# Kernel tuning notes

Measured on AMD Instinct MI355X. Metric: run time of the kernel, lower is better.

The kernel has to match this reference:

```python
import jax, jax.numpy as jnp
import numpy as np

V, N, K, D = 100000, 20000, 32, 128
NEG = -1e9  # masked logit value


def setup_inputs() -> dict:
    key = jax.random.key(0)
    ks = jax.random.split(key, 8)
    return {
        "nodes": jax.random.randint(ks[0], (N,), 0, V),
        "neigh_idx": jax.random.randint(ks[1], (N, K), 0, V),
        "degrees": jax.random.randint(ks[2], (N,), 0, K + 1),
        "u2e": jax.random.normal(ks[3], (V, D), dtype=jnp.float32),
        "W1": jax.random.normal(ks[4], (2 * D, D), dtype=jnp.float32) * 0.05,
        "b1": jnp.zeros((D,), jnp.float32),
        "W2": jax.random.normal(ks[5], (D, D), dtype=jnp.float32) * 0.05,
        "b2": jnp.zeros((D,), jnp.float32),
        "W3": jax.random.normal(ks[6], (D, 1), dtype=jnp.float32) * 0.05,
        "b3": jnp.zeros((1,), jnp.float32),
    }


def reference(nodes, neigh_idx, degrees, u2e, W1, b1, W2, b2, W3, b3):
    self_feats = u2e[nodes]                      # [N, D]
    e_u = u2e[neigh_idx]                         # [N, K, D] ragged gather (padded)
    # Attention MLP: cat(neighbor, self) -> relu -> relu -> scalar logit
    x = jnp.concatenate([e_u, jnp.broadcast_to(self_feats[:, None, :], (e_u.shape[0], K, D))], axis=-1)  # [N, K, 2D]
    h = jax.nn.relu(x @ W1 + b1)                 # [N, K, D]
    h = jax.nn.relu(h @ W2 + b2)                 # [N, K, D]
    logits = (h @ W3 + b3)[..., 0]               # [N, K]
    mask = jnp.arange(K)[None, :] < degrees[:, None]
    att = jax.nn.softmax(jnp.where(mask, logits, NEG), axis=-1)  # softmax over neighbors
    agg = jnp.einsum("nk,nkd->nd", att, e_u)     # attention-weighted neighbor sum
    out = jnp.where(degrees[:, None] > 0, (agg + self_feats) * 0.5, self_feats)
    return out
```

## Files before the change

kernel.cpp:

```cpp
#include <hip/hip_runtime.h>
#include <hip/hip_bf16.h>

#define KK 32
#define DD 128
#define NEGV (-1e9f)
#define SE 136

typedef __attribute__((ext_vector_type(8))) short bf16x8;
typedef __attribute__((ext_vector_type(4))) float f32x4;

__device__ __forceinline__ unsigned short f2bf(float f) {
    union { float f; unsigned u; } v; v.f = f;
    unsigned r = v.u + 0x7fffu + ((v.u >> 16) & 1u);
    return (unsigned short)(r >> 16);
}
__device__ __forceinline__ float bf2f(unsigned short h) {
    union { unsigned u; float f; } v; v.u = ((unsigned)h) << 16;
    return v.f;
}
__device__ __forceinline__ unsigned pk2(float x, float y) {
    union { __hip_bfloat162 h; unsigned u; } c;
    c.h = __float22bfloat162_rn(float2{x, y});
    return c.u;
}

__global__ __launch_bounds__(256) void prep_kernel(
    const float* __restrict__ u2e, const float* __restrict__ W1, const float* __restrict__ W2,
    unsigned short* __restrict__ u2e_bf, unsigned short* __restrict__ W1t,
    unsigned short* __restrict__ W2t, const int u2e_blocks)
{
    const int b = blockIdx.x;
    if (b < u2e_blocks) {
        const long base = (long)b * 2048 + threadIdx.x * 8;
        const float4* s = (const float4*)(u2e + base);
        const float4 v0 = s[0], v1 = s[1];
        uint4 p;
        p.x = pk2(v0.x, v0.y); p.y = pk2(v0.z, v0.w);
        p.z = pk2(v1.x, v1.y); p.w = pk2(v1.z, v1.w);
        *(uint4*)(u2e_bf + base) = p;
    } else {
        const int id = (b - u2e_blocks) * 256 + threadIdx.x;
        if (id < 256 * 128) {
            const int n = id >> 8, k = id & 255;
            W1t[id] = f2bf(W1[k * DD + n]);
        } else {
            const int j = id - 256 * 128;
            const int n = j >> 7, k = j & 127;
            W2t[j] = f2bf(W2[k * DD + n]);
        }
    }
}

template<bool BF>
__global__ __launch_bounds__(256, 2) void ppagg_mfma(
    const int* __restrict__ nodes, const int* __restrict__ neigh,
    const int* __restrict__ degrees, const float* __restrict__ u2e,
    const unsigned short* __restrict__ u2e_bf,
    const unsigned short* __restrict__ W1t, const unsigned short* __restrict__ W2t,
    const float* __restrict__ b1, const float* __restrict__ b2,
    const float* __restrict__ W3, const float* __restrict__ b3,
    float* __restrict__ out, const int Nn)
{
    __shared__ __align__(16) unsigned short s_eh[128 * SE];
    __shared__ __align__(16) unsigned short s_x[4 * DD];
    __shared__ float s_part[4][128];
    __shared__ float s_att[128];
    __shared__ int   s_idx[256];

    const int tid  = threadIdx.x;
    const int w    = tid >> 6;
    const int lane = tid & 63;
    const int ln   = lane & 15;
    const int q    = lane >> 4;

    bf16x8 b1f[8][2], b2f[4][2];
    float b1c[2], b2c[2], w3c[2];
    const int c0 = w * 32 + ln;
    const int c1 = c0 + 16;
    #pragma unroll
    for (int kk = 0; kk < 8; ++kk) {
        b1f[kk][0] = *(const bf16x8*)(W1t + c0 * 256 + kk * 32 + q * 8);
        b1f[kk][1] = *(const bf16x8*)(W1t + c1 * 256 + kk * 32 + q * 8);
    }
    #pragma unroll
    for (int kk = 0; kk < 4; ++kk) {
        b2f[kk][0] = *(const bf16x8*)(W2t + c0 * 128 + kk * 32 + q * 8);
        b2f[kk][1] = *(const bf16x8*)(W2t + c1 * 128 + kk * 32 + q * 8);
    }
    b1c[0] = b1[c0]; b1c[1] = b1[c1];
    b2c[0] = b2[c0]; b2c[1] = b2[c1];
    w3c[0] = W3[c0]; w3c[1] = W3[c1];

    const int nb = blockIdx.x * 8;
    const int r  = tid & 127;
    const int h  = tid >> 7;

    int idxA, idxB;
    {
        int ng0 = nb + (r >> 5);       if (ng0 >= Nn) ng0 = Nn - 1;
        int ng1 = nb + 4 + (r >> 5);   if (ng1 >= Nn) ng1 = Nn - 1;
        idxA = neigh[ng0 * KK + (r & 31)];
        idxB = neigh[ng1 * KK + (r & 31)];
    }
    float2 self0, self1;
    {
        int n0 = nb + w;       if (n0 >= Nn) n0 = Nn - 1;
        int n1 = nb + 4 + w;   if (n1 >= Nn) n1 = Nn - 1;
        self0 = *(const float2*)(u2e + (long)nodes[n0] * DD + lane * 2);
        self1 = *(const float2*)(u2e + (long)nodes[n1] * DD + lane * 2);
    }

    #pragma unroll
    for (int it = 0; it < 2; ++it) {
        const int gbase = nb + it * 4;
        const float2 selfv = it ? self1 : self0;
        const int myidx = it ? idxB : idxA;

        {
            unsigned short* dst = s_eh + r * SE + h * 64;
            if (BF) {
                const uint4* src = (const uint4*)(u2e_bf + (long)myidx * DD + h * 64);
                #pragma unroll
                for (int c = 0; c < 8; ++c) *(uint4*)(dst + c * 8) = src[c];
            } else {
                const float4* src = (const float4*)(u2e + (long)myidx * DD + h * 64);
                #pragma unroll
                for (int c8 = 0; c8 < 8; ++c8) {
                    const float4 v0 = src[c8 * 2];
                    const float4 v1 = src[c8 * 2 + 1];
                    uint4 p;
                    p.x = pk2(v0.x, v0.y); p.y = pk2(v0.z, v0.w);
                    p.z = pk2(v1.x, v1.y); p.w = pk2(v1.z, v1.w);
                    *(uint4*)(dst + c8 * 8) = p;
                }
            }
            *(unsigned*)(s_x + w * DD + lane * 2) = pk2(selfv.x, selfv.y);
            if (it == 0 && h == 0) { s_idx[r] = idxA; s_idx[128 + r] = idxB; }
        }
        __syncthreads();

        f32x4 acc[8][2];
        #pragma unroll
        for (int mt = 0; mt < 8; ++mt) {
            acc[mt][0] = (f32x4){0.f, 0.f, 0.f, 0.f};
            acc[mt][1] = (f32x4){0.f, 0.f, 0.f, 0.f};
        }
        #pragma unroll
        for (int kk = 0; kk < 4; ++kk) {
            bf16x8 a[8];
            #pragma unroll
            for (int mt = 0; mt < 8; ++mt)
                a[mt] = *(const bf16x8*)(s_eh + (mt * 16 + ln) * SE + kk * 32 + q * 8);
            #pragma unroll
            for (int mt = 0; mt < 8; ++mt) {
                acc[mt][0] = __builtin_amdgcn_mfma_f32_16x16x32_bf16(a[mt], b1f[kk][0], acc[mt][0], 0, 0, 0);
                acc[mt][1] = __builtin_amdgcn_mfma_f32_16x16x32_bf16(a[mt], b1f[kk][1], acc[mt][1], 0, 0, 0);
            }
        }
        #pragma unroll
        for (int kk = 4; kk < 8; ++kk) {
            #pragma unroll
            for (int mt = 0; mt < 8; ++mt) {
                const bf16x8 a = *(const bf16x8*)(s_x + (mt >> 1) * DD + (kk - 4) * 32 + q * 8);
                acc[mt][0] = __builtin_amdgcn_mfma_f32_16x16x32_bf16(a, b1f[kk][0], acc[mt][0], 0, 0, 0);
                acc[mt][1] = __builtin_amdgcn_mfma_f32_16x16x32_bf16(a, b1f[kk][1], acc[mt][1], 0, 0, 0);
            }
        }
        __syncthreads();

        #pragma unroll
        for (int mt = 0; mt < 8; ++mt)
            #pragma unroll
            for (int nt = 0; nt < 2; ++nt) {
                const int c = nt ? c1 : c0;
                #pragma unroll
                for (int rr = 0; rr < 4; rr += 2) {
                    const unsigned p = pk2(fmaxf(acc[mt][nt][rr]     + b1c[nt], 0.f),
                                           fmaxf(acc[mt][nt][rr + 1] + b1c[nt], 0.f));
                    const int row = mt * 16 + q * 4 + rr;
                    s_eh[row * SE + c]       = (unsigned short)(p & 0xffffu);
                    s_eh[(row + 1) * SE + c] = (unsigned short)(p >> 16);
                }
            }
        __syncthreads();

        f32x4 acc2[8][2];
        #pragma unroll
        for (int mt = 0; mt < 8; ++mt) {
            acc2[mt][0] = (f32x4){0.f, 0.f, 0.f, 0.f};
            acc2[mt][1] = (f32x4){0.f, 0.f, 0.f, 0.f};
        }
        #pragma unroll
        for (int kk = 0; kk < 4; ++kk) {
            bf16x8 a[8];
            #pragma unroll
            for (int mt = 0; mt < 8; ++mt)
                a[mt] = *(const bf16x8*)(s_eh + (mt * 16 + ln) * SE + kk * 32 + q * 8);
            #pragma unroll
            for (int mt = 0; mt < 8; ++mt) {
                acc2[mt][0] = __builtin_amdgcn_mfma_f32_16x16x32_bf16(a[mt], b2f[kk][0], acc2[mt][0], 0, 0, 0);
                acc2[mt][1] = __builtin_amdgcn_mfma_f32_16x16x32_bf16(a[mt], b2f[kk][1], acc2[mt][1], 0, 0, 0);
            }
        }
        #pragma unroll
        for (int mt = 0; mt < 8; ++mt) {
            float p[4];
            #pragma unroll
            for (int rr = 0; rr < 4; ++rr) {
                const float h0 = fmaxf(acc2[mt][0][rr] + b2c[0], 0.f);
                const float h1v = fmaxf(acc2[mt][1][rr] + b2c[1], 0.f);
                p[rr] = fmaf(h0, w3c[0], h1v * w3c[1]);
            }
            #pragma unroll
            for (int off = 1; off < 16; off <<= 1) {
                #pragma unroll
                for (int rr = 0; rr < 4; ++rr) p[rr] += __shfl_xor(p[rr], off);
            }
            if (ln == 0) {
                const int row0 = mt * 16 + q * 4;
                #pragma unroll
                for (int rr = 0; rr < 4; ++rr) s_part[w][row0 + rr] = p[rr];
            }
        }
        __syncthreads();

        if (tid < 128) {
            const int row = tid;
            const float logit = s_part[0][row] + s_part[1][row] + s_part[2][row] + s_part[3][row] + b3[0];
            int ng = gbase + (row >> 5);
            if (ng >= Nn) ng = Nn - 1;
            const int deg = degrees[ng];
            const float ml = ((row & 31) < deg) ? logit : NEGV;
            float mx = ml;
            #pragma unroll
            for (int off = 16; off > 0; off >>= 1) mx = fmaxf(mx, __shfl_xor(mx, off));
            const float e = __expf(ml - mx);
            float ssum = e;
            #pragma unroll
            for (int off = 16; off > 0; off >>= 1) ssum += __shfl_xor(ssum, off);
            s_att[row] = e / ssum;
        }
        __syncthreads();

        {
            const int ng = gbase + w;
            float ax = 0.f, ay = 0.f;
            #pragma unroll
            for (int k = 0; k < KK; ++k) {
                const float a    = s_att[w * KK + k];
                const int   ridx = s_idx[it * 128 + w * KK + k];
                if (BF) {
                    const unsigned pe = *(const unsigned*)(u2e_bf + (long)ridx * DD + lane * 2);
                    ax = fmaf(a, bf2f((unsigned short)(pe & 0xffffu)), ax);
                    ay = fmaf(a, bf2f((unsigned short)(pe >> 16)), ay);
                } else {
                    const float2 ev = *(const float2*)(u2e + (long)ridx * DD + lane * 2);
                    ax = fmaf(a, ev.x, ax);
                    ay = fmaf(a, ev.y, ay);
                }
            }
            if (ng < Nn) {
                const int deg = degrees[ng];
                float2 o;
                o.x = (deg > 0) ? 0.5f * (ax + selfv.x) : selfv.x;
                o.y = (deg > 0) ? 0.5f * (ay + selfv.y) : selfv.y;
                *(float2*)(out + (long)ng * DD + lane * 2) = o;
            }
        }
    }
}

extern "C" void kernel_launch(void* const* d_in, const int* in_sizes, int n_in,
                              void* d_out, int out_size, void* d_ws, size_t ws_size,
                              hipStream_t stream) {
    const int*   nodes   = (const int*)d_in[0];
    const int*   neigh   = (const int*)d_in[1];
    const int*   degrees = (const int*)d_in[2];
    const float* u2e     = (const float*)d_in[3];
    const float* W1      = (const float*)d_in[4];
    const float* b1      = (const float*)d_in[5];
    const float* W2      = (const float*)d_in[6];
    const float* b2      = (const float*)d_in[7];
    const float* W3      = (const float*)d_in[8];
    const float* b3      = (const float*)d_in[9];
    float* out = (float*)d_out;

    const int  Nn = in_sizes[0];
    const long Vd = (long)in_sizes[3];

    unsigned short* W1t = (unsigned short*)d_ws;
    unsigned short* W2t = W1t + 256 * 128;
    unsigned short* u2e_bf = W2t + 128 * 128;

    const size_t need_bf = (size_t)(256 * 128 + 128 * 128) * 2 + (size_t)Vd * 2;
    const bool use_bf = (ws_size >= need_bf) && (Vd % 2048 == 0);
    const int u2e_blocks = use_bf ? (int)(Vd / 2048) : 0;

    prep_kernel<<<u2e_blocks + 192, 256, 0, stream>>>(u2e, W1, W2, u2e_bf, W1t, W2t, u2e_blocks);

    const int grid = (Nn + 7) / 8;
    if (use_bf)
        ppagg_mfma<true><<<grid, 256, 0, stream>>>(nodes, neigh, degrees, u2e, u2e_bf,
                                                   W1t, W2t, b1, b2, W3, b3, out, Nn);
    else
        ppagg_mfma<false><<<grid, 256, 0, stream>>>(nodes, neigh, degrees, u2e, nullptr,
                                                    W1t, W2t, b1, b2, W3, b3, out, Nn);
}
```

Baseline: 216.6 us.

## Make MFMA aggregation kernel persistent with prefetch of next unit's indices

Replaces the fixed two-iteration-per-block scheme with a grid-stride persistent loop over 4-node units, capped at 1024 blocks. The neighbor indices and self features for the next unit are loaded into registers while the current unit's MLP runs, and double-buffered shared index storage keeps them separate. This amortizes the per-block weight-fragment loads into registers across many units and hides index-load latency. In exchange, the grid size is fixed, so load balance and occupancy now depend on the 1024 cap, and the loop is no longer unrolled.

```diff
diff --git a/kernel.cpp b/kernel.cpp
--- a/kernel.cpp
+++ b/kernel.cpp
@@ -65,7 +65,7 @@
     __shared__ __align__(16) unsigned short s_x[4 * DD];
     __shared__ float s_part[4][128];
     __shared__ float s_att[128];
-    __shared__ int   s_idx[256];
+    __shared__ int   s_idx[2][128];
 
     const int tid  = threadIdx.x;
     const int w    = tid >> 6;
@@ -91,39 +91,33 @@
     b2c[0] = b2[c0]; b2c[1] = b2[c1];
     w3c[0] = W3[c0]; w3c[1] = W3[c1];
 
-    const int nb = blockIdx.x * 8;
     const int r  = tid & 127;
     const int h  = tid >> 7;
 
-    int idxA, idxB;
+    const int units = (Nn + 3) / 4;
+    int u = blockIdx.x;
+
+    int idx_cur; float2 self_cur;
     {
-        int ng0 = nb + (r >> 5);       if (ng0 >= Nn) ng0 = Nn - 1;
-        int ng1 = nb + 4 + (r >> 5);   if (ng1 >= Nn) ng1 = Nn - 1;
-        idxA = neigh[ng0 * KK + (r & 31)];
-        idxB = neigh[ng1 * KK + (r & 31)];
-    }
-    float2 self0, self1;
-    {
-        int n0 = nb + w;       if (n0 >= Nn) n0 = Nn - 1;
-        int n1 = nb + 4 + w;   if (n1 >= Nn) n1 = Nn - 1;
-        self0 = *(const float2*)(u2e + (long)nodes[n0] * DD + lane * 2);
-        self1 = *(const float2*)(u2e + (long)nodes[n1] * DD + lane * 2);
-    }
-
-    #pragma unroll
-    for (int it = 0; it < 2; ++it) {
-        const int gbase = nb + it * 4;
-        const float2 selfv = it ? self1 : self0;
-        const int myidx = it ? idxB : idxA;
+        const int uc = (u < units) ? u : (units - 1);
+        int ng = uc * 4 + (r >> 5); if (ng >= Nn) ng = Nn - 1;
+        idx_cur = neigh[ng * KK + (r & 31)];
+        int ns = uc * 4 + w; if (ns >= Nn) ns = Nn - 1;
+        self_cur = *(const float2*)(u2e + (long)nodes[ns] * DD + lane * 2);
+    }
+
+    int par = 0;
+    for (; u < units; u += gridDim.x, par ^= 1) {
+        const int gbase = u * 4;
 
         {
             unsigned short* dst = s_eh + r * SE + h * 64;
             if (BF) {
-                const uint4* src = (const uint4*)(u2e_bf + (long)myidx * DD + h * 64);
+                const uint4* src = (const uint4*)(u2e_bf + (long)idx_cur * DD + h * 64);
                 #pragma unroll
                 for (int c = 0; c < 8; ++c) *(uint4*)(dst + c * 8) = src[c];
             } else {
-                const float4* src = (const float4*)(u2e + (long)myidx * DD + h * 64);
+                const float4* src = (const float4*)(u2e + (long)idx_cur * DD + h * 64);
                 #pragma unroll
                 for (int c8 = 0; c8 < 8; ++c8) {
                     const float4 v0 = src[c8 * 2];
@@ -134,10 +128,21 @@
                     *(uint4*)(dst + c8 * 8) = p;
                 }
             }
-            *(unsigned*)(s_x + w * DD + lane * 2) = pk2(selfv.x, selfv.y);
-            if (it == 0 && h == 0) { s_idx[r] = idxA; s_idx[128 + r] = idxB; }
-        }
-        __syncthreads();
+            *(unsigned*)(s_x + w * DD + lane * 2) = pk2(self_cur.x, self_cur.y);
+            if (h == 0) s_idx[par][r] = idx_cur;
+        }
+        __syncthreads();
+
+        int idx_next = idx_cur; float2 self_next = self_cur;
+        {
+            const int un = u + gridDim.x;
+            if (un < units) {
+                int ng = un * 4 + (r >> 5); if (ng >= Nn) ng = Nn - 1;
+                idx_next = neigh[ng * KK + (r & 31)];
+                int ns = un * 4 + w; if (ns >= Nn) ns = Nn - 1;
+                self_next = *(const float2*)(u2e + (long)nodes[ns] * DD + lane * 2);
+            }
+        }
 
         f32x4 acc[8][2];
         #pragma unroll
@@ -207,7 +212,7 @@
             float p[4];
             #pragma unroll
             for (int rr = 0; rr < 4; ++rr) {
-                const float h0 = fmaxf(acc2[mt][0][rr] + b2c[0], 0.f);
+                const float h0  = fmaxf(acc2[mt][0][rr] + b2c[0], 0.f);
                 const float h1v = fmaxf(acc2[mt][1][rr] + b2c[1], 0.f);
                 p[rr] = fmaf(h0, w3c[0], h1v * w3c[1]);
             }
@@ -248,7 +253,7 @@
             #pragma unroll
             for (int k = 0; k < KK; ++k) {
                 const float a    = s_att[w * KK + k];
-                const int   ridx = s_idx[it * 128 + w * KK + k];
+                const int   ridx = s_idx[par][w * KK + k];
                 if (BF) {
                     const unsigned pe = *(const unsigned*)(u2e_bf + (long)ridx * DD + lane * 2);
                     ax = fmaf(a, bf2f((unsigned short)(pe & 0xffffu)), ax);
@@ -262,11 +267,12 @@
             if (ng < Nn) {
                 const int deg = degrees[ng];
                 float2 o;
-                o.x = (deg > 0) ? 0.5f * (ax + selfv.x) : selfv.x;
-                o.y = (deg > 0) ? 0.5f * (ay + selfv.y) : selfv.y;
+                o.x = (deg > 0) ? 0.5f * (ax + self_cur.x) : self_cur.x;
+                o.y = (deg > 0) ? 0.5f * (ay + self_cur.y) : self_cur.y;
                 *(float2*)(out + (long)ng * DD + lane * 2) = o;
             }
         }
+        idx_cur = idx_next; self_cur = self_next;
     }
 }
 
@@ -298,7 +304,8 @@
 
     prep_kernel<<<u2e_blocks + 192, 256, 0, stream>>>(u2e, W1, W2, u2e_bf, W1t, W2t, u2e_blocks);
 
-    const int grid = (Nn + 7) / 8;
+    const int units = (Nn + 3) / 4;
+    const int grid  = units < 1024 ? units : 1024;
     if (use_bf)
         ppagg_mfma<true><<<grid, 256, 0, stream>>>(nodes, neigh, degrees, u2e, u2e_bf,
                                                    W1t, W2t, b1, b2, W3, b3, out, Nn);
```

Measured after the change: 235.2 us. 1.09x slower.

## Repartition second MLP layer per wave so softmax needs no cross-wave reduction

Applied to the files above, without the earlier changes.

Layer 2 is re-tiled so each wave computes all 128 output columns for the 32 neighbor rows of its own node, instead of a 32-column slice across all 128 rows. The logit dot product with W3 and the masked softmax can then finish inside one wave, which removes the shared partial-sum buffer and two block-wide barriers. Degrees are also loaded once up front rather than re-read. In exchange, W2 fragments are now read from global/L2 on every k-step instead of being held in registers. That frees VGPRs but adds load latency and traffic inside the MFMA loop.

```diff
diff --git a/kernel.cpp b/kernel.cpp
--- a/kernel.cpp
+++ b/kernel.cpp
@@ -63,9 +63,9 @@
 {
     __shared__ __align__(16) unsigned short s_eh[128 * SE];
     __shared__ __align__(16) unsigned short s_x[4 * DD];
-    __shared__ float s_part[4][128];
-    __shared__ float s_att[128];
-    __shared__ int   s_idx[256];
+    __shared__ float s_l[4][32];
+    __shared__ float s_att[4][32];
+    __shared__ int   s_idx[2][128];
 
     const int tid  = threadIdx.x;
     const int w    = tid >> 6;
@@ -73,8 +73,8 @@
     const int ln   = lane & 15;
     const int q    = lane >> 4;
 
-    bf16x8 b1f[8][2], b2f[4][2];
-    float b1c[2], b2c[2], w3c[2];
+    bf16x8 b1f[8][2];
+    float b1c[2];
     const int c0 = w * 32 + ln;
     const int c1 = c0 + 16;
     #pragma unroll
@@ -82,14 +82,14 @@
         b1f[kk][0] = *(const bf16x8*)(W1t + c0 * 256 + kk * 32 + q * 8);
         b1f[kk][1] = *(const bf16x8*)(W1t + c1 * 256 + kk * 32 + q * 8);
     }
+    b1c[0] = b1[c0]; b1c[1] = b1[c1];
+    float b2c8[8], w3c8[8];
     #pragma unroll
-    for (int kk = 0; kk < 4; ++kk) {
-        b2f[kk][0] = *(const bf16x8*)(W2t + c0 * 128 + kk * 32 + q * 8);
-        b2f[kk][1] = *(const bf16x8*)(W2t + c1 * 128 + kk * 32 + q * 8);
-    }
-    b1c[0] = b1[c0]; b1c[1] = b1[c1];
-    b2c[0] = b2[c0]; b2c[1] = b2[c1];
-    w3c[0] = W3[c0]; w3c[1] = W3[c1];
+    for (int nt = 0; nt < 8; ++nt) {
+        b2c8[nt] = b2[nt * 16 + ln];
+        w3c8[nt] = W3[nt * 16 + ln];
+    }
+    const float b3c = b3[0];
 
     const int nb = blockIdx.x * 8;
     const int r  = tid & 127;
@@ -103,11 +103,13 @@
         idxB = neigh[ng1 * KK + (r & 31)];
     }
     float2 self0, self1;
+    int dg0, dg1;
     {
         int n0 = nb + w;       if (n0 >= Nn) n0 = Nn - 1;
         int n1 = nb + 4 + w;   if (n1 >= Nn) n1 = Nn - 1;
         self0 = *(const float2*)(u2e + (long)nodes[n0] * DD + lane * 2);
         self1 = *(const float2*)(u2e + (long)nodes[n1] * DD + lane * 2);
+        dg0 = degrees[n0]; dg1 = degrees[n1];
     }
 
     #pragma unroll
@@ -115,6 +117,7 @@
         const int gbase = nb + it * 4;
         const float2 selfv = it ? self1 : self0;
         const int myidx = it ? idxB : idxA;
+        const int deg   = it ? dg1 : dg0;
 
         {
             unsigned short* dst = s_eh + r * SE + h * 64;
@@ -135,7 +138,7 @@
                 }
             }
             *(unsigned*)(s_x + w * DD + lane * 2) = pk2(selfv.x, selfv.y);
-            if (it == 0 && h == 0) { s_idx[r] = idxA; s_idx[128 + r] = idxB; }
+            if (h == 0) s_idx[it][r] = myidx;
         }
         __syncthreads();
 
@@ -184,71 +187,75 @@
             }
         __syncthreads();
 
-        f32x4 acc2[8][2];
-        #pragma unroll
-        for (int mt = 0; mt < 8; ++mt) {
-            acc2[mt][0] = (f32x4){0.f, 0.f, 0.f, 0.f};
-            acc2[mt][1] = (f32x4){0.f, 0.f, 0.f, 0.f};
-        }
+        f32x4 acc2[2][8];
+        #pragma unroll
+        for (int mt = 0; mt < 2; ++mt)
+            #pragma unroll
+            for (int nt = 0; nt < 8; ++nt)
+                acc2[mt][nt] = (f32x4){0.f, 0.f, 0.f, 0.f};
         #pragma unroll
         for (int kk = 0; kk < 4; ++kk) {
-            bf16x8 a[8];
-            #pragma unroll
-            for (int mt = 0; mt < 8; ++mt)
-                a[mt] = *(const bf16x8*)(s_eh + (mt * 16 + ln) * SE + kk * 32 + q * 8);
-            #pragma unroll
-            for (int mt = 0; mt < 8; ++mt) {
-                acc2[mt][0] = __builtin_amdgcn_mfma_f32_16x16x32_bf16(a[mt], b2f[kk][0], acc2[mt][0], 0, 0, 0);
-                acc2[mt][1] = __builtin_amdgcn_mfma_f32_16x16x32_bf16(a[mt], b2f[kk][1], acc2[mt][1], 0, 0, 0);
-            }
-        }
-        #pragma unroll
-        for (int mt = 0; mt < 8; ++mt) {
-            float p[4];
+            bf16x8 bs[8];
+            #pragma unroll
+            for (int nt = 0; nt < 8; ++nt)
+                bs[nt] = *(const bf16x8*)(W2t + (nt * 16 + ln) * 128 + kk * 32 + q * 8);
+            const bf16x8 a0 = *(const bf16x8*)(s_eh + (w * 32 + ln)      * SE + kk * 32 + q * 8);
+            const bf16x8 a1 = *(const bf16x8*)(s_eh + (w * 32 + 16 + ln) * SE + kk * 32 + q * 8);
+            #pragma unroll
+            for (int nt = 0; nt < 8; ++nt) {
+                acc2[0][nt] = __builtin_amdgcn_mfma_f32_16x16x32_bf16(a0, bs[nt], acc2[0][nt], 0, 0, 0);
+                acc2[1][nt] = __builtin_amdgcn_mfma_f32_16x16x32_bf16(a1, bs[nt], acc2[1][nt], 0, 0, 0);
+            }
+        }
+
+        float p[2][4];
+        #pragma unroll
+        for (int mt = 0; mt < 2; ++mt)
             #pragma unroll
             for (int rr = 0; rr < 4; ++rr) {
-                const float h0 = fmaxf(acc2[mt][0][rr] + b2c[0], 0.f);
-                const float h1v = fmaxf(acc2[mt][1][rr] + b2c[1], 0.f);
-                p[rr] = fmaf(h0, w3c[0], h1v * w3c[1]);
-            }
-            #pragma unroll
-            for (int off = 1; off < 16; off <<= 1) {
-                #pragma unroll
-                for (int rr = 0; rr < 4; ++rr) p[rr] += __shfl_xor(p[rr], off);
-            }
-            if (ln == 0) {
-                const int row0 = mt * 16 + q * 4;
-                #pragma unroll
-                for (int rr = 0; rr < 4; ++rr) s_part[w][row0 + rr] = p[rr];
-            }
-        }
-        __syncthreads();
-
-        if (tid < 128) {
-            const int row = tid;
-            const float logit = s_part[0][row] + s_part[1][row] + s_part[2][row] + s_part[3][row] + b3[0];
-            int ng = gbase + (row >> 5);
-            if (ng >= Nn) ng = Nn - 1;
-            const int deg = degrees[ng];
-            const float ml = ((row & 31) < deg) ? logit : NEGV;
+                float acc_p = 0.f;
+                #pragma unroll
+                for (int nt = 0; nt < 8; ++nt)
+                    acc_p = fmaf(fmaxf(acc2[mt][nt][rr] + b2c8[nt], 0.f), w3c8[nt], acc_p);
+                p[mt][rr] = acc_p;
+            }
+        #pragma unroll
+        for (int off = 1; off < 16; off <<= 1) {
+            #pragma unroll
+            for (int mt = 0; mt < 2; ++mt)
+                #pragma unroll
+                for (int rr = 0; rr < 4; ++rr)
+                    p[mt][rr] += __shfl_xor(p[mt][rr], off);
+        }
+        if (ln == 0) {
+            #pragma unroll
+            for (int mt = 0; mt < 2; ++mt)
+                #pragma unroll
+                for (int rr = 0; rr < 4; ++rr)
+                    s_l[w][mt * 16 + q * 4 + rr] = p[mt][rr];
+        }
+
+        {
+            const int k = lane & 31;
+            const float lg = s_l[w][k] + b3c;
+            const float ml = (k < deg) ? lg : NEGV;
             float mx = ml;
             #pragma unroll
-            for (int off = 16; off > 0; off >>= 1) mx = fmaxf(mx, __shfl_xor(mx, off));
+            for (int off = 1; off < 32; off <<= 1) mx = fmaxf(mx, __shfl_xor(mx, off));
             const float e = __expf(ml - mx);
             float ssum = e;
             #pragma unroll
-            for (int off = 16; off > 0; off >>= 1) ssum += __shfl_xor(ssum, off);
-            s_att[row] = e / ssum;
-        }
-        __syncthreads();
+            for (int off = 1; off < 32; off <<= 1) ssum += __shfl_xor(ssum, off);
+            if (lane < 32) s_att[w][lane] = e / ssum;
+        }
 
         {
             const int ng = gbase + w;
             float ax = 0.f, ay = 0.f;
             #pragma unroll
             for (int k = 0; k < KK; ++k) {
-                const float a    = s_att[w * KK + k];
-                const int   ridx = s_idx[it * 128 + w * KK + k];
+                const float a    = s_att[w][k];
+                const int   ridx = s_idx[it][w * KK + k];
                 if (BF) {
                     const unsigned pe = *(const unsigned*)(u2e_bf + (long)ridx * DD + lane * 2);
                     ax = fmaf(a, bf2f((unsigned short)(pe & 0xffffu)), ax);
@@ -260,13 +267,13 @@
                 }
             }
             if (ng < Nn) {
-                const int deg = degrees[ng];
                 float2 o;
                 o.x = (deg > 0) ? 0.5f * (ax + selfv.x) : selfv.x;
                 o.y = (deg > 0) ? 0.5f * (ay + selfv.y) : selfv.y;
                 *(float2*)(out + (long)ng * DD + lane * 2) = o;
             }
         }
+        __syncthreads();
     }
 }
 
```

Result: slower. 288.9 us (+33.3%).
